# Optimization experiments

Measured on AMD Instinct MI355X. Metric: run time of the kernel, lower is better.

The kernel has to match this reference:

```python
import jax, jax.numpy as jnp
import numpy as np

N_NODES = 100000
N_EDGES = 3200000
D_FEAT = 256
HIDDEN = 16


def setup_inputs() -> dict:
    key = jax.random.key(0)
    k1, k2, k3, k4 = jax.random.split(key, 4)
    x = jax.random.normal(k1, (N_NODES, D_FEAT), dtype=jnp.float32)
    edge_index = jax.random.randint(k2, (2, N_EDGES), 0, N_NODES, dtype=jnp.int64)
    # GCNConv linear weight (Glorot-ish scale) and bias
    W = jax.random.normal(k3, (D_FEAT, HIDDEN), dtype=jnp.float32) / np.sqrt(D_FEAT)
    b_conv = jnp.zeros((HIDDEN,), dtype=jnp.float32)
    W_fc = jax.random.normal(k4, (HIDDEN, 1), dtype=jnp.float32) / np.sqrt(HIDDEN)
    b_fc = jnp.zeros((1,), dtype=jnp.float32)
    return {"x": x, "edge_index": edge_index, "W": W, "b_conv": b_conv,
            "W_fc": W_fc, "b_fc": b_fc}


def reference(x, edge_index, W, b_conv, W_fc, b_fc):
    N = x.shape[0]
    # --- GCNConv: add self-loops, symmetric normalization, transform, scatter-add ---
    loop = jnp.arange(N, dtype=edge_index.dtype)
    src = jnp.concatenate([edge_index[0], loop])  # message sources (x_j)
    dst = jnp.concatenate([edge_index[1], loop])  # aggregation targets
    # degree of target nodes (edge weights = 1, self-loops included)
    deg = jax.ops.segment_sum(jnp.ones_like(dst, dtype=x.dtype), dst, num_segments=N)
    dinv = jnp.where(deg > 0, jax.lax.rsqrt(deg), 0.0)
    norm = dinv[src] * dinv[dst]  # [E+N]
    h = x @ W                       # [N, hidden] transform before propagation
    msg = h[src] * norm[:, None]    # gather + scale
    agg = jax.ops.segment_sum(msg, dst, num_segments=N)  # scatter-add
    out = agg + b_conv
    return out @ W_fc + b_fc
```

## Files before the change

kernel.cpp:

```cpp
#include <hip/hip_runtime.h>

#define DF 256
#define HID 16
#define WB 512
#define PBITS 8
#define PMAX 512
#define PPAD 512

__global__ void __launch_bounds__(512)
hist_sval_kernel(const float* __restrict__ x, const int* __restrict__ dst,
                 const float* __restrict__ Wm, const float* __restrict__ W_fc,
                 unsigned* __restrict__ cntS, float* __restrict__ sv,
                 int N, int E, int P, int Epw) {
    __shared__ unsigned h[PMAX];
    for (int i = threadIdx.x; i < P; i += 512) h[i] = 0u;
    __syncthreads();
    const int w = blockIdx.x;
    const size_t e0 = (size_t)w * Epw;
    long rem = (long)E - (long)e0;
    int m = rem < 0 ? 0 : (rem > Epw ? Epw : (int)rem);
    const int m4 = m >> 2;
    const int4* d4 = reinterpret_cast<const int4*>(dst + e0);
    for (int iv = threadIdx.x; iv < m4; iv += 512) {
        int4 d = d4[iv];
        atomicAdd(&h[((unsigned)d.x) >> PBITS], 1u);
        atomicAdd(&h[((unsigned)d.y) >> PBITS], 1u);
        atomicAdd(&h[((unsigned)d.z) >> PBITS], 1u);
        atomicAdd(&h[((unsigned)d.w) >> PBITS], 1u);
    }
    for (int i = (m4 << 2) + threadIdx.x; i < m; i += 512)
        atomicAdd(&h[((unsigned)dst[e0 + i]) >> PBITS], 1u);
    __syncthreads();
    for (int p = threadIdx.x; p < P; p += 512) cntS[(size_t)w * PPAD + p] = h[p];

    const int lane = threadIdx.x & 63, wid = threadIdx.x >> 6;
    const int gw = w * 8 + wid;
    const int GW = WB * 8;
    float a0 = 0.f, a1 = 0.f, a2 = 0.f, a3 = 0.f;
    {
        const float* wrow = Wm + (size_t)(lane * 4) * HID;
#pragma unroll
        for (int k = 0; k < HID; ++k) {
            float f = W_fc[k];
            a0 += wrow[k] * f;
            a1 += wrow[HID + k] * f;
            a2 += wrow[2 * HID + k] * f;
            a3 += wrow[3 * HID + k] * f;
        }
    }
    for (int r0 = gw; r0 < N; r0 += 4 * GW) {
        int r1 = r0 + GW, r2 = r0 + 2 * GW, r3 = r0 + 3 * GW;
        float4 v0, v1, v2, v3;
        v0 = reinterpret_cast<const float4*>(x + (size_t)r0 * DF)[lane];
        if (r1 < N) v1 = reinterpret_cast<const float4*>(x + (size_t)r1 * DF)[lane];
        if (r2 < N) v2 = reinterpret_cast<const float4*>(x + (size_t)r2 * DF)[lane];
        if (r3 < N) v3 = reinterpret_cast<const float4*>(x + (size_t)r3 * DF)[lane];
        float s0 = v0.x * a0 + v0.y * a1 + v0.z * a2 + v0.w * a3;
        float s1 = (r1 < N) ? (v1.x * a0 + v1.y * a1 + v1.z * a2 + v1.w * a3) : 0.f;
        float s2 = (r2 < N) ? (v2.x * a0 + v2.y * a1 + v2.z * a2 + v2.w * a3) : 0.f;
        float s3 = (r3 < N) ? (v3.x * a0 + v3.y * a1 + v3.z * a2 + v3.w * a3) : 0.f;
#pragma unroll
        for (int off = 32; off > 0; off >>= 1) {
            s0 += __shfl_xor(s0, off, 64);
            s1 += __shfl_xor(s1, off, 64);
            s2 += __shfl_xor(s2, off, 64);
            s3 += __shfl_xor(s3, off, 64);
        }
        if (lane == 0) {
            sv[r0] = s0;
            if (r1 < N) sv[r1] = s1;
            if (r2 < N) sv[r2] = s2;
            if (r3 < N) sv[r3] = s3;
        }
    }
}

__global__ void __launch_bounds__(WB)
rowscan_kernel(unsigned* __restrict__ cntS, unsigned* __restrict__ rowTotal, unsigned cap) {
    __shared__ unsigned wsum[8];
    const int p = blockIdx.x, t = threadIdx.x;
    const int lane = t & 63, wv = t >> 6;
    unsigned v = cntS[(size_t)t * PPAD + p];
    unsigned xi = v;
#pragma unroll
    for (int off = 1; off < 64; off <<= 1) {
        unsigned u = __shfl_up(xi, off, 64);
        if (lane >= off) xi += u;
    }
    if (lane == 63) wsum[wv] = xi;
    __syncthreads();
    if (t < 8) {
        unsigned u = wsum[t];
#pragma unroll
        for (int off = 1; off < 8; off <<= 1) {
            unsigned uu = __shfl_up(u, off, 64);
            if (t >= off) u += uu;
        }
        wsum[t] = u;
    }
    __syncthreads();
    unsigned base = wv ? wsum[wv - 1] : 0u;
    cntS[(size_t)t * PPAD + p] = xi - v + base + (unsigned)p * cap;
    if (t == 0) rowTotal[p] = wsum[7];
}

__global__ void __launch_bounds__(512)
binscatter_kernel(const int* __restrict__ src, const int* __restrict__ dst,
                  const unsigned* __restrict__ cntS, unsigned* __restrict__ sorted,
                  int P, int E, int Epw) {
    __shared__ unsigned cur[PMAX];
    const int w = blockIdx.x;
    for (int p = threadIdx.x; p < P; p += 512)
        cur[p] = cntS[(size_t)w * PPAD + p];
    __syncthreads();
    const size_t e0 = (size_t)w * Epw;
    long rem = (long)E - (long)e0;
    int m = rem < 0 ? 0 : (rem > Epw ? Epw : (int)rem);
    const int m4 = m >> 2;
    const int4* s4 = reinterpret_cast<const int4*>(src + e0);
    const int4* d4 = reinterpret_cast<const int4*>(dst + e0);
    for (int iv = threadIdx.x; iv < m4; iv += 512) {
        int4 s = s4[iv];
        int4 d = d4[iv];
        unsigned t0 = atomicAdd(&cur[((unsigned)d.x) >> PBITS], 1u);
        unsigned t1 = atomicAdd(&cur[((unsigned)d.y) >> PBITS], 1u);
        unsigned t2 = atomicAdd(&cur[((unsigned)d.z) >> PBITS], 1u);
        unsigned t3 = atomicAdd(&cur[((unsigned)d.w) >> PBITS], 1u);
        sorted[t0] = ((unsigned)s.x << PBITS) | ((unsigned)d.x & 255u);
        sorted[t1] = ((unsigned)s.y << PBITS) | ((unsigned)d.y & 255u);
        sorted[t2] = ((unsigned)s.z << PBITS) | ((unsigned)d.z & 255u);
        sorted[t3] = ((unsigned)s.w << PBITS) | ((unsigned)d.w & 255u);
    }
    for (int i = (m4 << 2) + threadIdx.x; i < m; i += 512) {
        unsigned s = (unsigned)src[e0 + i], d = (unsigned)dst[e0 + i];
        unsigned slot = atomicAdd(&cur[d >> PBITS], 1u);
        sorted[slot] = (s << PBITS) | (d & 255u);
    }
}

__global__ void __launch_bounds__(1024)
degfin_kernel(const unsigned* __restrict__ sorted, const unsigned* __restrict__ rowTotal,
              const float* __restrict__ sv, float* __restrict__ dinv,
              float* __restrict__ tval, int N, unsigned cap) {
    __shared__ unsigned dc[256];
    const int p = blockIdx.x, t = threadIdx.x;
    if (t < 256) dc[t] = 0u;
    __syncthreads();
    const unsigned cnt = rowTotal[p];
    const unsigned b0 = (unsigned)p * cap;
    const unsigned nv = cnt >> 2;
    const uint4* v4 = reinterpret_cast<const uint4*>(sorted + b0);
    for (unsigned iv = t; iv < nv; iv += 1024) {
        uint4 v = v4[iv];
        atomicAdd(&dc[v.x & 255u], 1u); atomicAdd(&dc[v.y & 255u], 1u);
        atomicAdd(&dc[v.z & 255u], 1u); atomicAdd(&dc[v.w & 255u], 1u);
    }
    for (unsigned j = (nv << 2) + t; j < cnt; j += 1024)
        atomicAdd(&dc[sorted[b0 + j] & 255u], 1u);
    __syncthreads();
    if (t < 256) {
        int i = (p << PBITS) + t;
        if (i < N) {
            float deg = 1.0f + (float)dc[t];
            float di = rsqrtf(deg);
            dinv[i] = di;
            tval[i] = sv[i] * di;
        }
    }
}

__global__ void __launch_bounds__(1024)
reduce_kernel(const unsigned* __restrict__ sorted, const unsigned* __restrict__ rowTotal,
              const float* __restrict__ tval, const float* __restrict__ dinv,
              const float* __restrict__ b_conv, const float* __restrict__ W_fc,
              const float* __restrict__ b_fc, float* __restrict__ out, int N, unsigned cap) {
    __shared__ float facc[256];
    const int p = blockIdx.x, t = threadIdx.x;
    if (t < 256) facc[t] = 0.f;
    __syncthreads();
    const unsigned cnt = rowTotal[p];
    const unsigned b0 = (unsigned)p * cap;
    const unsigned nv = cnt >> 2;
    const uint4* v4 = reinterpret_cast<const uint4*>(sorted + b0);
    for (unsigned iv = t; iv < nv; iv += 1024) {
        uint4 v = v4[iv];
        float f0 = tval[v.x >> PBITS], f1 = tval[v.y >> PBITS];
        float f2 = tval[v.z >> PBITS], f3 = tval[v.w >> PBITS];
        atomicAdd(&facc[v.x & 255u], f0); atomicAdd(&facc[v.y & 255u], f1);
        atomicAdd(&facc[v.z & 255u], f2); atomicAdd(&facc[v.w & 255u], f3);
    }
    for (unsigned j = (nv << 2) + t; j < cnt; j += 1024) {
        unsigned e = sorted[b0 + j];
        atomicAdd(&facc[e & 255u], tval[e >> PBITS]);
    }
    __syncthreads();
    if (t < 256) {
        int i = (p << PBITS) + t;
        if (i < N) {
            float c = 0.f;
#pragma unroll
            for (int k = 0; k < HID; ++k) c += b_conv[k] * W_fc[k];
            float di = dinv[i];
            out[i] = di * (tval[i] + facc[t]) + c + b_fc[0];
        }
    }
}

__global__ void fb_sval(const float* __restrict__ x, const float* __restrict__ Wm,
                        const float* __restrict__ W_fc, float* __restrict__ sv, int N) {
    __shared__ float wl[DF];
    int k = threadIdx.x;
    float a = 0.f;
#pragma unroll
    for (int j = 0; j < HID; ++j) a += Wm[k * HID + j] * W_fc[j];
    wl[k] = a;
    __syncthreads();
    int lane = threadIdx.x & 63, wid = threadIdx.x >> 6;
    float4 wv = reinterpret_cast<const float4*>(wl)[lane];
    for (int row = blockIdx.x * 4 + wid; row < N; row += gridDim.x * 4) {
        float4 xv = reinterpret_cast<const float4*>(x + (size_t)row * DF)[lane];
        float acc = xv.x * wv.x + xv.y * wv.y + xv.z * wv.z + xv.w * wv.w;
#pragma unroll
        for (int off = 32; off > 0; off >>= 1) acc += __shfl_xor(acc, off, 64);
        if (lane == 0) sv[row] = acc;
    }
}
__global__ void fb_count(const int* __restrict__ dst, unsigned* __restrict__ cnt, int E) {
    int stride = gridDim.x * blockDim.x;
    for (int e = blockIdx.x * blockDim.x + threadIdx.x; e < E; e += stride)
        atomicAdd(&cnt[dst[e]], 1u);
}
__global__ void fb_node(const unsigned* __restrict__ cnt, const float* __restrict__ sv,
                        const float* __restrict__ b_conv, const float* __restrict__ W_fc,
                        const float* __restrict__ b_fc, float* __restrict__ dinv,
                        float* __restrict__ tval, float* __restrict__ out, int N) {
    int i = blockIdx.x * blockDim.x + threadIdx.x;
    if (i < N) {
        float c = 0.f;
#pragma unroll
        for (int j = 0; j < HID; ++j) c += b_conv[j] * W_fc[j];
        float deg = 1.0f + (float)cnt[i];
        float di = rsqrtf(deg);
        float s = sv[i];
        dinv[i] = di; tval[i] = s * di;
        out[i] = s / deg + c + b_fc[0];
    }
}
__global__ void fb_scatter(const int* __restrict__ src, const int* __restrict__ dst,
                           const float* __restrict__ tval, const float* __restrict__ dinv,
                           float* __restrict__ out, int E) {
    int stride = gridDim.x * blockDim.x;
    for (int e = blockIdx.x * blockDim.x + threadIdx.x; e < E; e += stride) {
        int si = src[e], di = dst[e];
        atomicAdd(&out[di], tval[si] * dinv[di]);
    }
}

extern "C" void kernel_launch(void* const* d_in, const int* in_sizes, int n_in,
                              void* d_out, int out_size, void* d_ws, size_t ws_size,
                              hipStream_t stream) {
    const float* x      = (const float*)d_in[0];
    const int*   ei     = (const int*)d_in[1];
    const float* Wm     = (const float*)d_in[2];
    const float* b_conv = (const float*)d_in[3];
    const float* W_fc   = (const float*)d_in[4];
    const float* b_fc   = (const float*)d_in[5];
    float* out = (float*)d_out;

    const int N = in_sizes[0] / DF;
    const int E = in_sizes[1] / 2;
    const int* src = ei;
    const int* dst = ei + E;

    const int P   = (N + 255) >> PBITS;
    const int Epw = (((E + WB - 1) / WB) + 3) & ~3;
    const unsigned avg = (unsigned)((E + P - 1) / P);
    const unsigned cap = ((4u * avg) + 4095u) & ~4095u;

    char* ws = (char*)d_ws;
    float* sv   = (float*)ws;
    float* dinv = sv + N;
    float* tval = dinv + N;
    unsigned* cntS     = (unsigned*)(tval + N);
    unsigned* rowTotal = cntS + (size_t)WB * PPAD;
    unsigned* sorted   = rowTotal + 512;

    const size_t need = ((size_t)3 * N + (size_t)WB * PPAD + 512 + (size_t)P * cap) * 4;

    if (P >= 1 && P <= PMAX && N <= (1 << 23) && ws_size >= need) {
        hist_sval_kernel<<<WB, 512, 0, stream>>>(x, dst, Wm, W_fc, cntS, sv, N, E, P, Epw);
        rowscan_kernel<<<P, WB, 0, stream>>>(cntS, rowTotal, cap);
        binscatter_kernel<<<WB, 512, 0, stream>>>(src, dst, cntS, sorted, P, E, Epw);
        degfin_kernel<<<P, 1024, 0, stream>>>(sorted, rowTotal, sv, dinv, tval, N, cap);
        reduce_kernel<<<P, 1024, 0, stream>>>(sorted, rowTotal, tval, dinv,
                                              b_conv, W_fc, b_fc, out, N, cap);
    } else {
        unsigned* fcnt = (unsigned*)(tval + N);
        hipMemsetAsync(fcnt, 0, (size_t)N * 4, stream);
        fb_sval<<<2048, 256, 0, stream>>>(x, Wm, W_fc, sv, N);
        fb_count<<<2048, 256, 0, stream>>>(dst, fcnt, E);
        fb_node<<<(N + 255) / 256, 256, 0, stream>>>(fcnt, sv, b_conv, W_fc, b_fc, dinv, tval, out, N);
        fb_scatter<<<2048, 256, 0, stream>>>(src, dst, tval, dinv, out, E);
    }
}
```

Before: 82.79 us.

## Fuse scan, bin-scatter, degree and reduce into one persistent kernel with grid barriers

Merges the rowscan, binscatter, degree-finalize and reduce stages into one persistent 512-block kernel, separated by atomic-counter grid barriers. This removes three kernel launches and their drain gaps. The histogram kernel is also split so two waves build the dst histogram while six waves compute the projected node values concurrently. The grid barrier needs all blocks co-resident, which is checked with an occupancy query; if that fails it falls back to the multi-kernel path. The generic fallback path was removed.

```diff
diff --git a/kernel.cpp b/kernel.cpp
--- a/kernel.cpp
+++ b/kernel.cpp
@@ -3,9 +3,22 @@
 #define DF 256
 #define HID 16
 #define WB 512
+#define NBLK 512
 #define PBITS 8
 #define PMAX 512
 #define PPAD 512
+
+__device__ __forceinline__ void gbar(unsigned* cnt, unsigned target) {
+    __syncthreads();
+    if (threadIdx.x == 0) {
+        __hip_atomic_fetch_add(cnt, 1u, __ATOMIC_RELEASE, __HIP_MEMORY_SCOPE_AGENT);
+        unsigned it = 0;
+        while (__hip_atomic_load(cnt, __ATOMIC_ACQUIRE, __HIP_MEMORY_SCOPE_AGENT) < target
+               && ++it < (1u << 26))
+            __builtin_amdgcn_s_sleep(2);
+    }
+    __syncthreads();
+}
 
 __global__ void __launch_bounds__(512)
 hist_sval_kernel(const float* __restrict__ x, const int* __restrict__ dst,
@@ -15,29 +28,27 @@
     __shared__ unsigned h[PMAX];
     for (int i = threadIdx.x; i < P; i += 512) h[i] = 0u;
     __syncthreads();
-    const int w = blockIdx.x;
-    const size_t e0 = (size_t)w * Epw;
-    long rem = (long)E - (long)e0;
-    int m = rem < 0 ? 0 : (rem > Epw ? Epw : (int)rem);
-    const int m4 = m >> 2;
-    const int4* d4 = reinterpret_cast<const int4*>(dst + e0);
-    for (int iv = threadIdx.x; iv < m4; iv += 512) {
-        int4 d = d4[iv];
-        atomicAdd(&h[((unsigned)d.x) >> PBITS], 1u);
-        atomicAdd(&h[((unsigned)d.y) >> PBITS], 1u);
-        atomicAdd(&h[((unsigned)d.z) >> PBITS], 1u);
-        atomicAdd(&h[((unsigned)d.w) >> PBITS], 1u);
-    }
-    for (int i = (m4 << 2) + threadIdx.x; i < m; i += 512)
-        atomicAdd(&h[((unsigned)dst[e0 + i]) >> PBITS], 1u);
-    __syncthreads();
-    for (int p = threadIdx.x; p < P; p += 512) cntS[(size_t)w * PPAD + p] = h[p];
-
-    const int lane = threadIdx.x & 63, wid = threadIdx.x >> 6;
-    const int gw = w * 8 + wid;
-    const int GW = WB * 8;
-    float a0 = 0.f, a1 = 0.f, a2 = 0.f, a3 = 0.f;
-    {
+    const int w = blockIdx.x, tid = threadIdx.x;
+    if (tid < 128) {
+        const size_t e0 = (size_t)w * Epw;
+        long rem = (long)E - (long)e0;
+        int m = rem < 0 ? 0 : (rem > Epw ? Epw : (int)rem);
+        const int m4 = m >> 2;
+        const int4* d4 = reinterpret_cast<const int4*>(dst + e0);
+        for (int iv = tid; iv < m4; iv += 128) {
+            int4 d = d4[iv];
+            atomicAdd(&h[((unsigned)d.x) >> PBITS], 1u);
+            atomicAdd(&h[((unsigned)d.y) >> PBITS], 1u);
+            atomicAdd(&h[((unsigned)d.z) >> PBITS], 1u);
+            atomicAdd(&h[((unsigned)d.w) >> PBITS], 1u);
+        }
+        for (int i = (m4 << 2) + tid; i < m; i += 128)
+            atomicAdd(&h[((unsigned)dst[e0 + i]) >> PBITS], 1u);
+    } else {
+        const int lane = tid & 63, swid = (tid >> 6) - 2;
+        const int gw = w * 6 + swid;
+        const int GW = WB * 6;
+        float a0 = 0.f, a1 = 0.f, a2 = 0.f, a3 = 0.f;
         const float* wrow = Wm + (size_t)(lane * 4) * HID;
 #pragma unroll
         for (int k = 0; k < HID; ++k) {
@@ -47,30 +58,165 @@
             a2 += wrow[2 * HID + k] * f;
             a3 += wrow[3 * HID + k] * f;
         }
-    }
-    for (int r0 = gw; r0 < N; r0 += 4 * GW) {
-        int r1 = r0 + GW, r2 = r0 + 2 * GW, r3 = r0 + 3 * GW;
-        float4 v0, v1, v2, v3;
-        v0 = reinterpret_cast<const float4*>(x + (size_t)r0 * DF)[lane];
-        if (r1 < N) v1 = reinterpret_cast<const float4*>(x + (size_t)r1 * DF)[lane];
-        if (r2 < N) v2 = reinterpret_cast<const float4*>(x + (size_t)r2 * DF)[lane];
-        if (r3 < N) v3 = reinterpret_cast<const float4*>(x + (size_t)r3 * DF)[lane];
-        float s0 = v0.x * a0 + v0.y * a1 + v0.z * a2 + v0.w * a3;
-        float s1 = (r1 < N) ? (v1.x * a0 + v1.y * a1 + v1.z * a2 + v1.w * a3) : 0.f;
-        float s2 = (r2 < N) ? (v2.x * a0 + v2.y * a1 + v2.z * a2 + v2.w * a3) : 0.f;
-        float s3 = (r3 < N) ? (v3.x * a0 + v3.y * a1 + v3.z * a2 + v3.w * a3) : 0.f;
-#pragma unroll
-        for (int off = 32; off > 0; off >>= 1) {
-            s0 += __shfl_xor(s0, off, 64);
-            s1 += __shfl_xor(s1, off, 64);
-            s2 += __shfl_xor(s2, off, 64);
-            s3 += __shfl_xor(s3, off, 64);
-        }
-        if (lane == 0) {
-            sv[r0] = s0;
-            if (r1 < N) sv[r1] = s1;
-            if (r2 < N) sv[r2] = s2;
-            if (r3 < N) sv[r3] = s3;
+        for (int r0 = gw; r0 < N; r0 += 4 * GW) {
+            int r1 = r0 + GW, r2 = r0 + 2 * GW, r3 = r0 + 3 * GW;
+            float4 v0, v1, v2, v3;
+            v0 = reinterpret_cast<const float4*>(x + (size_t)r0 * DF)[lane];
+            if (r1 < N) v1 = reinterpret_cast<const float4*>(x + (size_t)r1 * DF)[lane];
+            if (r2 < N) v2 = reinterpret_cast<const float4*>(x + (size_t)r2 * DF)[lane];
+            if (r3 < N) v3 = reinterpret_cast<const float4*>(x + (size_t)r3 * DF)[lane];
+            float s0 = v0.x * a0 + v0.y * a1 + v0.z * a2 + v0.w * a3;
+            float s1 = (r1 < N) ? (v1.x * a0 + v1.y * a1 + v1.z * a2 + v1.w * a3) : 0.f;
+            float s2 = (r2 < N) ? (v2.x * a0 + v2.y * a1 + v2.z * a2 + v2.w * a3) : 0.f;
+            float s3 = (r3 < N) ? (v3.x * a0 + v3.y * a1 + v3.z * a2 + v3.w * a3) : 0.f;
+#pragma unroll
+            for (int off = 32; off > 0; off >>= 1) {
+                s0 += __shfl_xor(s0, off, 64);
+                s1 += __shfl_xor(s1, off, 64);
+                s2 += __shfl_xor(s2, off, 64);
+                s3 += __shfl_xor(s3, off, 64);
+            }
+            if (lane == 0) {
+                sv[r0] = s0;
+                if (r1 < N) sv[r1] = s1;
+                if (r2 < N) sv[r2] = s2;
+                if (r3 < N) sv[r3] = s3;
+            }
+        }
+    }
+    __syncthreads();
+    for (int p = threadIdx.x; p < P; p += 512) cntS[(size_t)w * PPAD + p] = h[p];
+}
+
+__global__ void __launch_bounds__(512, 4)
+fused_kernel(const int* __restrict__ src, const int* __restrict__ dst,
+             unsigned* __restrict__ cntS, unsigned* __restrict__ rowTotal,
+             unsigned* __restrict__ sorted, const float* __restrict__ sv,
+             float* __restrict__ dinv, float* __restrict__ tval,
+             const float* __restrict__ b_conv, const float* __restrict__ W_fc,
+             const float* __restrict__ b_fc, float* __restrict__ out,
+             unsigned* __restrict__ bars, int N, int E, int P, int Epw, unsigned cap) {
+    __shared__ unsigned wsum[8];
+    __shared__ unsigned cur[PMAX];
+    __shared__ unsigned dc[256];
+    __shared__ float facc[256];
+    const int t = threadIdx.x;
+
+    if (blockIdx.x < (unsigned)P) {
+        const int p = blockIdx.x;
+        const int lane = t & 63, wv = t >> 6;
+        unsigned v = cntS[(size_t)t * PPAD + p];
+        unsigned xi = v;
+#pragma unroll
+        for (int off = 1; off < 64; off <<= 1) {
+            unsigned u = __shfl_up(xi, off, 64);
+            if (lane >= off) xi += u;
+        }
+        if (lane == 63) wsum[wv] = xi;
+        __syncthreads();
+        if (t < 8) {
+            unsigned u = wsum[t];
+#pragma unroll
+            for (int off = 1; off < 8; off <<= 1) {
+                unsigned uu = __shfl_up(u, off, 64);
+                if (t >= off) u += uu;
+            }
+            wsum[t] = u;
+        }
+        __syncthreads();
+        unsigned base = wv ? wsum[wv - 1] : 0u;
+        cntS[(size_t)t * PPAD + p] = xi - v + base + (unsigned)p * cap;
+        if (t == 0) rowTotal[p] = wsum[7];
+    }
+    gbar(&bars[0], NBLK);
+
+    {
+        const int w = blockIdx.x;
+        for (int p = t; p < P; p += 512) cur[p] = cntS[(size_t)w * PPAD + p];
+        __syncthreads();
+        const size_t e0 = (size_t)w * Epw;
+        long rem = (long)E - (long)e0;
+        int m = rem < 0 ? 0 : (rem > Epw ? Epw : (int)rem);
+        const int m4 = m >> 2;
+        const int4* s4 = reinterpret_cast<const int4*>(src + e0);
+        const int4* d4 = reinterpret_cast<const int4*>(dst + e0);
+        for (int iv = t; iv < m4; iv += 512) {
+            int4 s = s4[iv];
+            int4 d = d4[iv];
+            unsigned t0 = atomicAdd(&cur[((unsigned)d.x) >> PBITS], 1u);
+            unsigned t1 = atomicAdd(&cur[((unsigned)d.y) >> PBITS], 1u);
+            unsigned t2 = atomicAdd(&cur[((unsigned)d.z) >> PBITS], 1u);
+            unsigned t3 = atomicAdd(&cur[((unsigned)d.w) >> PBITS], 1u);
+            sorted[t0] = ((unsigned)s.x << PBITS) | ((unsigned)d.x & 255u);
+            sorted[t1] = ((unsigned)s.y << PBITS) | ((unsigned)d.y & 255u);
+            sorted[t2] = ((unsigned)s.z << PBITS) | ((unsigned)d.z & 255u);
+            sorted[t3] = ((unsigned)s.w << PBITS) | ((unsigned)d.w & 255u);
+        }
+        for (int i = (m4 << 2) + t; i < m; i += 512) {
+            unsigned s = (unsigned)src[e0 + i], d = (unsigned)dst[e0 + i];
+            unsigned slot = atomicAdd(&cur[d >> PBITS], 1u);
+            sorted[slot] = (s << PBITS) | (d & 255u);
+        }
+    }
+    gbar(&bars[1], NBLK);
+
+    if (blockIdx.x < (unsigned)P) {
+        const int p = blockIdx.x;
+        if (t < 256) dc[t] = 0u;
+        __syncthreads();
+        const unsigned cnt = rowTotal[p];
+        const unsigned b0 = (unsigned)p * cap;
+        const unsigned nv = cnt >> 2;
+        const uint4* v4 = reinterpret_cast<const uint4*>(sorted + b0);
+        for (unsigned iv = t; iv < nv; iv += 512) {
+            uint4 v = v4[iv];
+            atomicAdd(&dc[v.x & 255u], 1u); atomicAdd(&dc[v.y & 255u], 1u);
+            atomicAdd(&dc[v.z & 255u], 1u); atomicAdd(&dc[v.w & 255u], 1u);
+        }
+        for (unsigned j = (nv << 2) + t; j < cnt; j += 512)
+            atomicAdd(&dc[sorted[b0 + j] & 255u], 1u);
+        __syncthreads();
+        if (t < 256) {
+            int i = (p << PBITS) + t;
+            if (i < N) {
+                float deg = 1.0f + (float)dc[t];
+                float di = rsqrtf(deg);
+                dinv[i] = di;
+                tval[i] = sv[i] * di;
+            }
+        }
+    }
+    gbar(&bars[2], NBLK);
+
+    if (blockIdx.x < (unsigned)P) {
+        const int p = blockIdx.x;
+        if (t < 256) facc[t] = 0.f;
+        __syncthreads();
+        const unsigned cnt = rowTotal[p];
+        const unsigned b0 = (unsigned)p * cap;
+        const unsigned nv = cnt >> 2;
+        const uint4* v4 = reinterpret_cast<const uint4*>(sorted + b0);
+        for (unsigned iv = t; iv < nv; iv += 512) {
+            uint4 v = v4[iv];
+            float f0 = tval[v.x >> PBITS], f1 = tval[v.y >> PBITS];
+            float f2 = tval[v.z >> PBITS], f3 = tval[v.w >> PBITS];
+            atomicAdd(&facc[v.x & 255u], f0); atomicAdd(&facc[v.y & 255u], f1);
+            atomicAdd(&facc[v.z & 255u], f2); atomicAdd(&facc[v.w & 255u], f3);
+        }
+        for (unsigned j = (nv << 2) + t; j < cnt; j += 512) {
+            unsigned e = sorted[b0 + j];
+            atomicAdd(&facc[e & 255u], tval[e >> PBITS]);
+        }
+        __syncthreads();
+        if (t < 256) {
+            int i = (p << PBITS) + t;
+            if (i < N) {
+                float c = 0.f;
+#pragma unroll
+                for (int k = 0; k < HID; ++k) c += b_conv[k] * W_fc[k];
+                float di = dinv[i];
+                out[i] = di * (tval[i] + facc[t]) + c + b_fc[0];
+            }
         }
     }
 }
@@ -103,15 +249,13 @@
     cntS[(size_t)t * PPAD + p] = xi - v + base + (unsigned)p * cap;
     if (t == 0) rowTotal[p] = wsum[7];
 }
-
 __global__ void __launch_bounds__(512)
 binscatter_kernel(const int* __restrict__ src, const int* __restrict__ dst,
                   const unsigned* __restrict__ cntS, unsigned* __restrict__ sorted,
                   int P, int E, int Epw) {
     __shared__ unsigned cur[PMAX];
     const int w = blockIdx.x;
-    for (int p = threadIdx.x; p < P; p += 512)
-        cur[p] = cntS[(size_t)w * PPAD + p];
+    for (int p = threadIdx.x; p < P; p += 512) cur[p] = cntS[(size_t)w * PPAD + p];
     __syncthreads();
     const size_t e0 = (size_t)w * Epw;
     long rem = (long)E - (long)e0;
@@ -137,7 +281,6 @@
         sorted[slot] = (s << PBITS) | (d & 255u);
     }
 }
-
 __global__ void __launch_bounds__(1024)
 degfin_kernel(const unsigned* __restrict__ sorted, const unsigned* __restrict__ rowTotal,
               const float* __restrict__ sv, float* __restrict__ dinv,
@@ -168,7 +311,6 @@
         }
     }
 }
-
 __global__ void __launch_bounds__(1024)
 reduce_kernel(const unsigned* __restrict__ sorted, const unsigned* __restrict__ rowTotal,
               const float* __restrict__ tval, const float* __restrict__ dinv,
@@ -206,56 +348,6 @@
     }
 }
 
-__global__ void fb_sval(const float* __restrict__ x, const float* __restrict__ Wm,
-                        const float* __restrict__ W_fc, float* __restrict__ sv, int N) {
-    __shared__ float wl[DF];
-    int k = threadIdx.x;
-    float a = 0.f;
-#pragma unroll
-    for (int j = 0; j < HID; ++j) a += Wm[k * HID + j] * W_fc[j];
-    wl[k] = a;
-    __syncthreads();
-    int lane = threadIdx.x & 63, wid = threadIdx.x >> 6;
-    float4 wv = reinterpret_cast<const float4*>(wl)[lane];
-    for (int row = blockIdx.x * 4 + wid; row < N; row += gridDim.x * 4) {
-        float4 xv = reinterpret_cast<const float4*>(x + (size_t)row * DF)[lane];
-        float acc = xv.x * wv.x + xv.y * wv.y + xv.z * wv.z + xv.w * wv.w;
-#pragma unroll
-        for (int off = 32; off > 0; off >>= 1) acc += __shfl_xor(acc, off, 64);
-        if (lane == 0) sv[row] = acc;
-    }
-}
-__global__ void fb_count(const int* __restrict__ dst, unsigned* __restrict__ cnt, int E) {
-    int stride = gridDim.x * blockDim.x;
-    for (int e = blockIdx.x * blockDim.x + threadIdx.x; e < E; e += stride)
-        atomicAdd(&cnt[dst[e]], 1u);
-}
-__global__ void fb_node(const unsigned* __restrict__ cnt, const float* __restrict__ sv,
-                        const float* __restrict__ b_conv, const float* __restrict__ W_fc,
-                        const float* __restrict__ b_fc, float* __restrict__ dinv,
-                        float* __restrict__ tval, float* __restrict__ out, int N) {
-    int i = blockIdx.x * blockDim.x + threadIdx.x;
-    if (i < N) {
-        float c = 0.f;
-#pragma unroll
-        for (int j = 0; j < HID; ++j) c += b_conv[j] * W_fc[j];
-        float deg = 1.0f + (float)cnt[i];
-        float di = rsqrtf(deg);
-        float s = sv[i];
-        dinv[i] = di; tval[i] = s * di;
-        out[i] = s / deg + c + b_fc[0];
-    }
-}
-__global__ void fb_scatter(const int* __restrict__ src, const int* __restrict__ dst,
-                           const float* __restrict__ tval, const float* __restrict__ dinv,
-                           float* __restrict__ out, int E) {
-    int stride = gridDim.x * blockDim.x;
-    for (int e = blockIdx.x * blockDim.x + threadIdx.x; e < E; e += stride) {
-        int si = src[e], di = dst[e];
-        atomicAdd(&out[di], tval[si] * dinv[di]);
-    }
-}
-
 extern "C" void kernel_launch(void* const* d_in, const int* in_sizes, int n_in,
                               void* d_out, int out_size, void* d_ws, size_t ws_size,
                               hipStream_t stream) {
@@ -278,28 +370,37 @@
     const unsigned cap = ((4u * avg) + 4095u) & ~4095u;
 
     char* ws = (char*)d_ws;
-    float* sv   = (float*)ws;
+    unsigned* bars = (unsigned*)ws;
+    float* sv   = (float*)(ws + 64);
     float* dinv = sv + N;
     float* tval = dinv + N;
     unsigned* cntS     = (unsigned*)(tval + N);
     unsigned* rowTotal = cntS + (size_t)WB * PPAD;
     unsigned* sorted   = rowTotal + 512;
 
-    const size_t need = ((size_t)3 * N + (size_t)WB * PPAD + 512 + (size_t)P * cap) * 4;
-
-    if (P >= 1 && P <= PMAX && N <= (1 << 23) && ws_size >= need) {
+    const size_t need = 64 + ((size_t)3 * N + (size_t)WB * PPAD + 512 + (size_t)P * cap) * 4;
+    const bool shape_ok = (P >= 1 && P <= PMAX && N <= (1 << 23) && ws_size >= need);
+
+    int maxBlocksPerCU = 0, numCU = 0;
+    bool occ_ok = false;
+    if (shape_ok &&
+        hipOccupancyMaxActiveBlocksPerMultiprocessor(&maxBlocksPerCU, fused_kernel, 512, 0)
+            == hipSuccess &&
+        hipDeviceGetAttribute(&numCU, hipDeviceAttributeMultiprocessorCount, 0) == hipSuccess)
+        occ_ok = ((long)maxBlocksPerCU * numCU >= NBLK);
+
+    if (shape_ok && occ_ok) {
+        hipMemsetAsync(bars, 0, 64, stream);
+        hist_sval_kernel<<<WB, 512, 0, stream>>>(x, dst, Wm, W_fc, cntS, sv, N, E, P, Epw);
+        fused_kernel<<<NBLK, 512, 0, stream>>>(src, dst, cntS, rowTotal, sorted, sv,
+                                               dinv, tval, b_conv, W_fc, b_fc, out, bars,
+                                               N, E, P, Epw, cap);
+    } else if (shape_ok) {
         hist_sval_kernel<<<WB, 512, 0, stream>>>(x, dst, Wm, W_fc, cntS, sv, N, E, P, Epw);
         rowscan_kernel<<<P, WB, 0, stream>>>(cntS, rowTotal, cap);
         binscatter_kernel<<<WB, 512, 0, stream>>>(src, dst, cntS, sorted, P, E, Epw);
         degfin_kernel<<<P, 1024, 0, stream>>>(sorted, rowTotal, sv, dinv, tval, N, cap);
         reduce_kernel<<<P, 1024, 0, stream>>>(sorted, rowTotal, tval, dinv,
                                               b_conv, W_fc, b_fc, out, N, cap);
-    } else {
-        unsigned* fcnt = (unsigned*)(tval + N);
-        hipMemsetAsync(fcnt, 0, (size_t)N * 4, stream);
-        fb_sval<<<2048, 256, 0, stream>>>(x, Wm, W_fc, sv, N);
-        fb_count<<<2048, 256, 0, stream>>>(dst, fcnt, E);
-        fb_node<<<(N + 255) / 256, 256, 0, stream>>>(fcnt, sv, b_conv, W_fc, b_fc, dinv, tval, out, N);
-        fb_scatter<<<2048, 256, 0, stream>>>(src, dst, tval, dinv, out, E);
-    }
-}
+    }
+}
```

Result: slower. 306.5 us (+270.2%).
